# Kernel tuning notes

Hardware: AMD Instinct MI355X
Metric: run time of the kernel (lower is better)

## Reference

```python
import jax, jax.numpy as jnp
import numpy as np

N = 27          # num_classes (nodes)
C = 512         # in_channels
B = 64          # batch
L = 2           # layer_num
EPS = 1e-5


def setup_inputs() -> dict:
    key = jax.random.key(0)
    ks = jax.random.split(key, 7)
    scale = (2.0 / C) ** 0.5  # matches weight.data.normal_(0, sqrt(2/in_channels))
    mk = lambda k: jax.random.normal(k, (L, C, C), jnp.float32) * scale
    return {
        "x": jax.random.normal(ks[0], (B, N, C), jnp.float32),
        "edge": jax.random.normal(ks[1], (B, N * N, C), jnp.float32),
        "Wu": mk(ks[2]),
        "Wv": mk(ks[3]),
        "Wa": mk(ks[4]),
        "Wb": mk(ks[5]),
        "We": mk(ks[6]),
        "bnv_w": jnp.ones((L, N), jnp.float32),
        "bnv_b": jnp.zeros((L, N), jnp.float32),
        "bne_w": jnp.ones((L, N * N), jnp.float32),
        "bne_b": jnp.zeros((L, N * N), jnp.float32),
    }


def _bn(t, w, b):
    # BatchNorm1d in training mode over [B, channels, C]-style layout:
    # input is [B, ch, C]; normalize over (batch, last) dims, biased variance.
    mean = jnp.mean(t, axis=(0, 2), keepdims=True)
    var = jnp.mean((t - mean) ** 2, axis=(0, 2), keepdims=True)
    return (t - mean) * jax.lax.rsqrt(var + EPS) * w[None, :, None] + b[None, :, None]


def _layer(x, edge, Wu, Wv, Wa, Wb, We, bnv_w, bnv_b, bne_w, bne_b):
    b = x.shape[0]
    # einsum('ev,bvc->bec', end, A(x)) == repeat each node i over its n outgoing rows
    Ax = jnp.repeat(x @ Wa.T, N, axis=1)            # [b, n*n, c]
    # einsum('ev,bvc->bec', start, B(x)) == tile all nodes n times
    Bx = jnp.tile(x @ Wb.T, (1, N, 1))              # [b, n*n, c]
    m = Ax + Bx + edge @ We.T
    edge = edge + jax.nn.relu(_bn(m, bne_w, bne_b))
    e = jax.nn.sigmoid(edge)
    # softmax over dim 2 of the [b, n, n, c] view
    e = jax.nn.softmax(e.reshape(b, N, N, C), axis=2).reshape(b, N * N, C)
    Ujx = jnp.tile(x @ Wv.T, (1, N, 1))             # start-gather of V(x)
    # einsum('ve,bec->bvc', end.T, .) == segment-sum over consecutive groups of n edges
    agg = (e * Ujx).reshape(b, N, N, C).sum(axis=2)  # [b, n, c]
    x = x @ Wu.T + agg / N
    x = x + jax.nn.relu(_bn(x, bnv_w, bnv_b))
    return x, edge


def reference(x, edge, Wu, Wv, Wa, Wb, We, bnv_w, bnv_b, bne_w, bne_b):
    for l in range(L):
        x, edge = _layer(x, edge, Wu[l], Wv[l], Wa[l], Wb[l], We[l],
                         bnv_w[l], bnv_b[l], bne_w[l], bne_b[l])
    return (x, edge)
```

## Files before the change

kernel.cpp:

```cpp
#include <hip/hip_runtime.h>
#include <math.h>

#define NN 27
#define NE 729
#define CC 512
#define BB 64
#define EPSV 1e-5f

#define XROWS (BB*NN)
#define EROWS (BB*NE)

typedef short s16x8 __attribute__((ext_vector_type(8)));
typedef float f32x4 __attribute__((ext_vector_type(4)));
typedef unsigned short bfu_t;

typedef const __attribute__((address_space(1))) void gv_t;
typedef __attribute__((address_space(3))) void lv_t;

static __device__ __forceinline__ bfu_t f2bu(float f) {
    __bf16 h = (__bf16)f;
    return __builtin_bit_cast(unsigned short, h);
}

__global__ __launch_bounds__(256)
void f2b(const float* __restrict__ src, bfu_t* __restrict__ dst, int n)
{
    int i = (blockIdx.x * 256 + threadIdx.x) * 8;
    if (i >= n) return;
    float4 a = *(const float4*)(src + i);
    float4 b = *(const float4*)(src + i + 4);
    s16x8 v;
    v[0] = (short)f2bu(a.x); v[1] = (short)f2bu(a.y);
    v[2] = (short)f2bu(a.z); v[3] = (short)f2bu(a.w);
    v[4] = (short)f2bu(b.x); v[5] = (short)f2bu(b.y);
    v[6] = (short)f2bu(b.z); v[7] = (short)f2bu(b.w);
    *(s16x8*)(dst + i) = v;
}

__global__ __launch_bounds__(256)
void gemm_mfma(const bfu_t* __restrict__ A, const bfu_t* __restrict__ W,
               float* __restrict__ out, int M, int ldo,
               const float* __restrict__ xW, int mode)
{
    __shared__ bfu_t As[128 * 32];
    __shared__ bfu_t Bs[128 * 32];

    const int t    = threadIdx.x;
    const int lane = t & 63;
    const int w    = t >> 6;
    const int bm   = blockIdx.x * 128;
    const int bn   = blockIdx.y * 128;
    const int wr   = (w >> 1) * 64;
    const int wc   = (w & 1) * 64;

    f32x4 acc[4][4];
    #pragma unroll
    for (int i = 0; i < 4; ++i)
        #pragma unroll
        for (int j = 0; j < 4; ++j) acc[i][j] = (f32x4){0.f, 0.f, 0.f, 0.f};

    const int r0 = w * 32 + (lane >> 2);
    const int r1 = r0 + 16;
    const int kc = (lane & 3) * 8;
    int ga0 = bm + r0; if (ga0 > M - 1) ga0 = M - 1;
    int ga1 = bm + r1; if (ga1 > M - 1) ga1 = M - 1;
    const bfu_t* a0 = A + (size_t)ga0 * CC + kc;
    const bfu_t* a1 = A + (size_t)ga1 * CC + kc;
    const bfu_t* w0 = W + (size_t)(bn + r0) * CC + kc;
    const bfu_t* w1 = W + (size_t)(bn + r1) * CC + kc;
    bfu_t* lA0 = As + (w * 2 + 0) * 512;
    bfu_t* lA1 = As + (w * 2 + 1) * 512;
    bfu_t* lB0 = Bs + (w * 2 + 0) * 512;
    bfu_t* lB1 = Bs + (w * 2 + 1) * 512;

    const int fra = wr + (lane & 15);
    const int frb = wc + (lane & 15);
    const int fk  = (lane >> 4) * 8;

    for (int kt = 0; kt < CC; kt += 32) {
        if (kt) __syncthreads();
        __builtin_amdgcn_global_load_lds((gv_t*)(a0 + kt), (lv_t*)lA0, 16, 0, 0);
        __builtin_amdgcn_global_load_lds((gv_t*)(a1 + kt), (lv_t*)lA1, 16, 0, 0);
        __builtin_amdgcn_global_load_lds((gv_t*)(w0 + kt), (lv_t*)lB0, 16, 0, 0);
        __builtin_amdgcn_global_load_lds((gv_t*)(w1 + kt), (lv_t*)lB1, 16, 0, 0);
        __syncthreads();

        s16x8 af[4], bfg[4];
        #pragma unroll
        for (int i = 0; i < 4; ++i)
            af[i] = *(const s16x8*)&As[(fra + i * 16) * 32 + fk];
        #pragma unroll
        for (int i = 0; i < 4; ++i)
            bfg[i] = *(const s16x8*)&Bs[(frb + i * 16) * 32 + fk];
        #pragma unroll
        for (int i = 0; i < 4; ++i)
            #pragma unroll
            for (int j = 0; j < 4; ++j)
                acc[i][j] = __builtin_amdgcn_mfma_f32_16x16x32_bf16(af[i], bfg[j], acc[i][j], 0, 0, 0);
    }

    const int crb = wr + ((lane >> 4) << 2);
    const int ccb = wc + (lane & 15);
    if (mode == 0) {
        #pragma unroll
        for (int mi = 0; mi < 4; ++mi) {
            #pragma unroll
            for (int q = 0; q < 4; ++q) {
                int row = bm + crb + mi * 16 + q;
                if (row >= M) continue;
                float* o = out + (size_t)row * ldo + bn + ccb;
                #pragma unroll
                for (int ni = 0; ni < 4; ++ni) o[ni * 16] = acc[mi][ni][q];
            }
        }
    } else {
        #pragma unroll
        for (int mi = 0; mi < 4; ++mi) {
            #pragma unroll
            for (int q = 0; q < 4; ++q) {
                int row = bm + crb + mi * 16 + q;
                if (row >= M) continue;
                int b  = row / NE;
                int e  = row - b * NE;
                int i2 = e / NN;
                int j2 = e - i2 * NN;
                const float* axp = xW + (size_t)(b * NN + i2) * 2048 + bn + ccb;
                const float* bxp = xW + (size_t)(b * NN + j2) * 2048 + 512 + bn + ccb;
                float* o = out + (size_t)row * CC + bn + ccb;
                #pragma unroll
                for (int ni = 0; ni < 4; ++ni)
                    o[ni * 16] = acc[mi][ni][q] + axp[ni * 16] + bxp[ni * 16];
            }
        }
    }
}

__global__ __launch_bounds__(256)
void bn_stats(const float* __restrict__ src, int nch,
              const float* __restrict__ w, const float* __restrict__ bias,
              float* __restrict__ ka, float* __restrict__ kb)
{
    const int ch = blockIdx.x;
    const int t  = threadIdx.x;
    const int sub = t >> 7;
    const int cf  = (t & 127) * 4;

    float s = 0.f, sq = 0.f;
    for (int b = 0; b < BB; b += 2) {
        const float* p = src + ((size_t)(b + sub) * nch + ch) * CC + cf;
        float4 v = *(const float4*)p;
        s  += v.x + v.y + v.z + v.w;
        sq += v.x*v.x + v.y*v.y + v.z*v.z + v.w*v.w;
    }
    #pragma unroll
    for (int off = 32; off; off >>= 1) {
        s  += __shfl_down(s, off);
        sq += __shfl_down(sq, off);
    }
    __shared__ float red[2][4];
    const int wid = t >> 6, lane = t & 63;
    if (lane == 0) { red[0][wid] = s; red[1][wid] = sq; }
    __syncthreads();
    if (t == 0) {
        s  = red[0][0] + red[0][1] + red[0][2] + red[0][3];
        sq = red[1][0] + red[1][1] + red[1][2] + red[1][3];
        const float inv = 1.f / (float)(BB * CC);
        float mean = s * inv;
        float var  = sq * inv - mean * mean;
        float r    = rsqrtf(var + EPSV);
        float kaw  = r * w[ch];
        ka[ch] = kaw;
        kb[ch] = bias[ch] - mean * kaw;
    }
}

__global__ __launch_bounds__(256)
void edge_update(const float* __restrict__ m, const float* __restrict__ ein,
                 float* __restrict__ eout, bfu_t* __restrict__ ebf,
                 const float* __restrict__ ka, const float* __restrict__ kb)
{
    const size_t idx = (size_t)blockIdx.x * blockDim.x + threadIdx.x;
    const size_t total = (size_t)EROWS * CC / 4;
    if (idx >= total) return;
    const int e = (int)((idx >> 7) % NE);
    const float a = ka[e], b = kb[e];
    float4 mv = ((const float4*)m)[idx];
    float4 ev = ((const float4*)ein)[idx];
    float4 o;
    o.x = ev.x + fmaxf(fmaf(mv.x, a, b), 0.f);
    o.y = ev.y + fmaxf(fmaf(mv.y, a, b), 0.f);
    o.z = ev.z + fmaxf(fmaf(mv.z, a, b), 0.f);
    o.w = ev.w + fmaxf(fmaf(mv.w, a, b), 0.f);
    ((float4*)eout)[idx] = o;
    ushort4 h;
    h.x = f2bu(o.x); h.y = f2bu(o.y); h.z = f2bu(o.z); h.w = f2bu(o.w);
    ((ushort4*)ebf)[idx] = h;
}

__global__ __launch_bounds__(512)
void agg_kernel(const float* __restrict__ edge, const float* __restrict__ xW,
                float* __restrict__ xpre)
{
    const int bi = blockIdx.x;
    const int c  = threadIdx.x;
    const int b  = bi / NN;
    const int i  = bi - b * NN;

    const float* ebase = edge + ((size_t)b * NE + (size_t)i * NN) * CC + c;
    float ex[NN];
    float den = 0.f;
    #pragma unroll
    for (int j = 0; j < NN; ++j) {
        float sv  = ebase[(size_t)j * CC];
        float sig = 1.f / (1.f + __expf(-sv));
        float e   = __expf(sig);
        ex[j] = e;
        den  += e;
    }
    float accv = 0.f;
    const float* vbase = xW + (size_t)(b * NN) * 2048 + 1024 + c;
    #pragma unroll
    for (int j = 0; j < NN; ++j)
        accv = fmaf(ex[j], vbase[(size_t)j * 2048], accv);

    float u = xW[(size_t)bi * 2048 + 1536 + c];
    xpre[(size_t)bi * CC + c] = u + accv / (den * (float)NN);
}

__global__ __launch_bounds__(256)
void x_update(const float* __restrict__ xpre, float* __restrict__ xout,
              bfu_t* __restrict__ xbf,
              const float* __restrict__ ka, const float* __restrict__ kb)
{
    const int idx = blockIdx.x * blockDim.x + threadIdx.x;
    const int total = XROWS * CC / 4;
    if (idx >= total) return;
    const int i = (idx >> 7) % NN;
    const float a = ka[i], b = kb[i];
    float4 v = ((const float4*)xpre)[idx];
    float4 o;
    o.x = v.x + fmaxf(fmaf(v.x, a, b), 0.f);
    o.y = v.y + fmaxf(fmaf(v.y, a, b), 0.f);
    o.z = v.z + fmaxf(fmaf(v.z, a, b), 0.f);
    o.w = v.w + fmaxf(fmaf(v.w, a, b), 0.f);
    ((float4*)xout)[idx] = o;
    ushort4 h;
    h.x = f2bu(o.x); h.y = f2bu(o.y); h.z = f2bu(o.z); h.w = f2bu(o.w);
    ((ushort4*)xbf)[idx] = h;
}

extern "C" void kernel_launch(void* const* d_in, const int* in_sizes, int n_in,
                              void* d_out, int out_size, void* d_ws, size_t ws_size,
                              hipStream_t stream)
{
    const float* x0   = (const float*)d_in[0];
    const float* e0   = (const float*)d_in[1];
    const float* Wu   = (const float*)d_in[2];
    const float* Wv   = (const float*)d_in[3];
    const float* Wa   = (const float*)d_in[4];
    const float* Wb   = (const float*)d_in[5];
    const float* We   = (const float*)d_in[6];
    const float* bnvw = (const float*)d_in[7];
    const float* bnvb = (const float*)d_in[8];
    const float* bnew = (const float*)d_in[9];
    const float* bneb = (const float*)d_in[10];

    const size_t XSZ = (size_t)XROWS * CC;
    const size_t ESZ = (size_t)EROWS * CC;
    const int    WSZ = CC * CC;

    float* xout = (float*)d_out;
    float* eout = xout + XSZ;

    float* ws   = (float*)d_ws;
    float* xW   = ws;
    float* m    = xW + (size_t)XROWS * 2048;
    float* xpre = m + ESZ;
    float* ka_e = xpre + XSZ;
    float* kb_e = ka_e + NE;
    float* ka_v = kb_e + NE;
    float* kb_v = ka_v + NN;
    bfu_t* bws  = (bfu_t*)(ka_v + 2048);
    bfu_t* ebf  = bws;
    bfu_t* xbf  = ebf + ESZ;
    bfu_t* WnB  = xbf + XSZ;
    bfu_t* WeB  = WnB + (size_t)2 * 2048 * CC;

    const int wgrid = WSZ / 8 / 256;
    for (int l = 0; l < 2; ++l) {
        bfu_t* nb = WnB + (size_t)l * 2048 * CC;
        f2b<<<wgrid, 256, 0, stream>>>(Wa + (size_t)l * WSZ, nb,            WSZ);
        f2b<<<wgrid, 256, 0, stream>>>(Wb + (size_t)l * WSZ, nb + WSZ,      WSZ);
        f2b<<<wgrid, 256, 0, stream>>>(Wv + (size_t)l * WSZ, nb + 2 * WSZ,  WSZ);
        f2b<<<wgrid, 256, 0, stream>>>(Wu + (size_t)l * WSZ, nb + 3 * WSZ,  WSZ);
        f2b<<<wgrid, 256, 0, stream>>>(We + (size_t)l * WSZ, WeB + (size_t)l * WSZ, WSZ);
    }

    const dim3 gN(14, 16);
    const dim3 gE(365, 4);

    for (int l = 0; l < 2; ++l) {
        const float* ei = l ? (const float*)eout : e0;
        if (l == 0) {
            f2b<<<(int)(XSZ / 8 / 256), 256, 0, stream>>>(x0, xbf, (int)XSZ);
            f2b<<<(int)(ESZ / 8 / 256), 256, 0, stream>>>(e0, ebf, (int)ESZ);
        }

        gemm_mfma<<<gN, 256, 0, stream>>>(xbf, WnB + (size_t)l * 2048 * CC,
                                          xW, XROWS, 2048, nullptr, 0);
        gemm_mfma<<<gE, 256, 0, stream>>>(ebf, WeB + (size_t)l * WSZ,
                                          m, EROWS, CC, xW, 1);

        bn_stats<<<NE, 256, 0, stream>>>(m, NE, bnew + (size_t)l * NE,
                                         bneb + (size_t)l * NE, ka_e, kb_e);
        edge_update<<<(int)(ESZ / 4 / 256), 256, 0, stream>>>(m, ei, eout, ebf, ka_e, kb_e);

        agg_kernel<<<XROWS, 512, 0, stream>>>(eout, xW, xpre);

        bn_stats<<<NN, 256, 0, stream>>>(xpre, NN, bnvw + (size_t)l * NN,
                                         bnvb + (size_t)l * NN, ka_v, kb_v);
        x_update<<<(int)(XSZ / 4 / 256), 256, 0, stream>>>(xpre, xout, xbf, ka_v, kb_v);
    }
}
```

Baseline: 572.0 us.

## Fuse BN statistics into GEMM epilogue and merge edge update with aggregation

Edge BatchNorm sums and sums of squares are now accumulated with atomics inside the edge GEMM epilogue, which removes the separate bn_stats pass over the large m tensor. The edge update (BN, relu, residual, bf16 copy) is fused into the softmax-aggregation kernel, so the new edge is consumed straight from registers instead of being re-read. Node BN statistics are likewise accumulated with atomics in that kernel and turned into scale and shift inside x_update. All bf16 conversions are merged into one launch. The atomics add contention and make float summation order nondeterministic.

Result: slower. 642.7 us (+12.4%).

```diff
diff --git a/kernel.cpp b/kernel.cpp
--- a/kernel.cpp
+++ b/kernel.cpp
@@ -6,14 +6,13 @@
 #define CC 512
 #define BB 64
 #define EPSV 1e-5f
-
 #define XROWS (BB*NN)
 #define EROWS (BB*NE)
+#define WSZ   (CC*CC)
 
 typedef short s16x8 __attribute__((ext_vector_type(8)));
 typedef float f32x4 __attribute__((ext_vector_type(4)));
 typedef unsigned short bfu_t;
-
 typedef const __attribute__((address_space(1))) void gv_t;
 typedef __attribute__((address_space(3))) void lv_t;
 
@@ -23,24 +22,58 @@
 }
 
 __global__ __launch_bounds__(256)
-void f2b(const float* __restrict__ src, bfu_t* __restrict__ dst, int n)
-{
-    int i = (blockIdx.x * 256 + threadIdx.x) * 8;
-    if (i >= n) return;
-    float4 a = *(const float4*)(src + i);
-    float4 b = *(const float4*)(src + i + 4);
+void zero_stats(float* __restrict__ p)
+{
+    p[blockIdx.x * 256 + threadIdx.x] = 0.f;
+}
+
+__global__ __launch_bounds__(256)
+void convert_all(const float* __restrict__ Wa, const float* __restrict__ Wb,
+                 const float* __restrict__ Wv, const float* __restrict__ Wu,
+                 const float* __restrict__ We, const float* __restrict__ x0,
+                 const float* __restrict__ e0,
+                 bfu_t* __restrict__ WnB, bfu_t* __restrict__ WeB,
+                 bfu_t* __restrict__ xbf, bfu_t* __restrict__ ebf)
+{
+    const long i = (long)(blockIdx.x * 256 + threadIdx.x) * 8;
+    const long WTOT = 10L * WSZ;
+    const long XTOT = WTOT + (long)XROWS * CC;
+    const float* src;
+    bfu_t* dst;
+    if (i < WTOT) {
+        int  c   = (int)(i >> 18);
+        long off = i & (WSZ - 1);
+        if (c < 8) {
+            int l = c >> 2, t = c & 3;
+            const float* b = (t == 0) ? Wa : (t == 1) ? Wb : (t == 2) ? Wv : Wu;
+            src = b + (long)l * WSZ + off;
+            dst = WnB + (long)c * WSZ + off;
+        } else {
+            src = We + (long)(c - 8) * WSZ + off;
+            dst = WeB + (long)(c - 8) * WSZ + off;
+        }
+    } else if (i < XTOT) {
+        long off = i - WTOT;
+        src = x0 + off;  dst = xbf + off;
+    } else {
+        long off = i - XTOT;
+        src = e0 + off;  dst = ebf + off;
+    }
+    float4 a = *(const float4*)src;
+    float4 b = *(const float4*)(src + 4);
     s16x8 v;
     v[0] = (short)f2bu(a.x); v[1] = (short)f2bu(a.y);
     v[2] = (short)f2bu(a.z); v[3] = (short)f2bu(a.w);
     v[4] = (short)f2bu(b.x); v[5] = (short)f2bu(b.y);
     v[6] = (short)f2bu(b.z); v[7] = (short)f2bu(b.w);
-    *(s16x8*)(dst + i) = v;
+    *(s16x8*)dst = v;
 }
 
 __global__ __launch_bounds__(256)
 void gemm_mfma(const bfu_t* __restrict__ A, const bfu_t* __restrict__ W,
                float* __restrict__ out, int M, int ldo,
-               const float* __restrict__ xW, int mode)
+               const float* __restrict__ xW, int mode,
+               float* __restrict__ esum, float* __restrict__ esumsq)
 {
     __shared__ bfu_t As[128 * 32];
     __shared__ bfu_t Bs[128 * 32];
@@ -127,116 +160,120 @@
                 const float* axp = xW + (size_t)(b * NN + i2) * 2048 + bn + ccb;
                 const float* bxp = xW + (size_t)(b * NN + j2) * 2048 + 512 + bn + ccb;
                 float* o = out + (size_t)row * CC + bn + ccb;
+                float s = 0.f, sq = 0.f;
                 #pragma unroll
-                for (int ni = 0; ni < 4; ++ni)
-                    o[ni * 16] = acc[mi][ni][q] + axp[ni * 16] + bxp[ni * 16];
+                for (int ni = 0; ni < 4; ++ni) {
+                    float v = acc[mi][ni][q] + axp[ni * 16] + bxp[ni * 16];
+                    o[ni * 16] = v;
+                    s += v; sq += v * v;
+                }
+                #pragma unroll
+                for (int off = 1; off < 16; off <<= 1) {
+                    s  += __shfl_xor(s, off);
+                    sq += __shfl_xor(sq, off);
+                }
+                if ((lane & 15) == 0) {
+                    atomicAdd(&esum[e], s);
+                    atomicAdd(&esumsq[e], sq);
+                }
             }
         }
     }
 }
 
 __global__ __launch_bounds__(256)
-void bn_stats(const float* __restrict__ src, int nch,
-              const float* __restrict__ w, const float* __restrict__ bias,
-              float* __restrict__ ka, float* __restrict__ kb)
-{
-    const int ch = blockIdx.x;
-    const int t  = threadIdx.x;
-    const int sub = t >> 7;
-    const int cf  = (t & 127) * 4;
-
-    float s = 0.f, sq = 0.f;
-    for (int b = 0; b < BB; b += 2) {
-        const float* p = src + ((size_t)(b + sub) * nch + ch) * CC + cf;
-        float4 v = *(const float4*)p;
-        s  += v.x + v.y + v.z + v.w;
-        sq += v.x*v.x + v.y*v.y + v.z*v.z + v.w*v.w;
-    }
+void agg_edge(const float* __restrict__ m, const float* __restrict__ ein,
+              float* __restrict__ eout, bfu_t* __restrict__ ebf,
+              const float* __restrict__ xW, float* __restrict__ xpre,
+              const float* __restrict__ esum, const float* __restrict__ esumsq,
+              const float* __restrict__ bnew, const float* __restrict__ bneb,
+              float* __restrict__ vsum, float* __restrict__ vsumsq)
+{
+    const int bi = blockIdx.x;
+    const int b  = bi / NN;
+    const int i  = bi - b * NN;
+    const int c  = threadIdx.x * 2;
+
+    __shared__ float kae[NN], kbe[NN];
+    if (threadIdx.x < NN) {
+        int e = i * NN + threadIdx.x;
+        const float inv = 1.f / (float)(BB * CC);
+        float mean = esum[e] * inv;
+        float var  = esumsq[e] * inv - mean * mean;
+        float r    = rsqrtf(var + EPSV);
+        float a    = r * bnew[e];
+        kae[threadIdx.x] = a;
+        kbe[threadIdx.x] = bneb[e] - mean * a;
+    }
+    __syncthreads();
+
+    const size_t ebase = ((size_t)b * NE + (size_t)i * NN) * CC + c;
+    float2 ex[NN];
+    float2 den = {0.f, 0.f};
+    #pragma unroll
+    for (int j = 0; j < NN; ++j) {
+        size_t idx = ebase + (size_t)j * CC;
+        float2 mv = *(const float2*)(m + idx);
+        float2 ev = *(const float2*)(ein + idx);
+        float a = kae[j], bb = kbe[j];
+        float2 o;
+        o.x = ev.x + fmaxf(fmaf(mv.x, a, bb), 0.f);
+        o.y = ev.y + fmaxf(fmaf(mv.y, a, bb), 0.f);
+        *(float2*)(eout + idx) = o;
+        ushort2 h; h.x = f2bu(o.x); h.y = f2bu(o.y);
+        *(ushort2*)(ebf + idx) = h;
+        float sx = 1.f / (1.f + __expf(-o.x));
+        float sy = 1.f / (1.f + __expf(-o.y));
+        float gx = __expf(sx), gy = __expf(sy);
+        ex[j].x = gx; ex[j].y = gy;
+        den.x += gx; den.y += gy;
+    }
+
+    float2 accv = {0.f, 0.f};
+    const float* vb = xW + (size_t)(b * NN) * 2048 + 1024 + c;
+    #pragma unroll
+    for (int j = 0; j < NN; ++j) {
+        float2 v = *(const float2*)(vb + (size_t)j * 2048);
+        accv.x = fmaf(ex[j].x, v.x, accv.x);
+        accv.y = fmaf(ex[j].y, v.y, accv.y);
+    }
+    float2 u = *(const float2*)(xW + (size_t)bi * 2048 + 1536 + c);
+    float2 xp;
+    xp.x = u.x + accv.x / (den.x * (float)NN);
+    xp.y = u.y + accv.y / (den.y * (float)NN);
+    *(float2*)(xpre + (size_t)bi * CC + c) = xp;
+
+    float s  = xp.x + xp.y;
+    float sq = xp.x * xp.x + xp.y * xp.y;
     #pragma unroll
     for (int off = 32; off; off >>= 1) {
         s  += __shfl_down(s, off);
         sq += __shfl_down(sq, off);
     }
-    __shared__ float red[2][4];
-    const int wid = t >> 6, lane = t & 63;
-    if (lane == 0) { red[0][wid] = s; red[1][wid] = sq; }
+    __shared__ float rs[4], rq[4];
+    const int wid = threadIdx.x >> 6, lane = threadIdx.x & 63;
+    if (lane == 0) { rs[wid] = s; rq[wid] = sq; }
     __syncthreads();
-    if (t == 0) {
-        s  = red[0][0] + red[0][1] + red[0][2] + red[0][3];
-        sq = red[1][0] + red[1][1] + red[1][2] + red[1][3];
-        const float inv = 1.f / (float)(BB * CC);
-        float mean = s * inv;
-        float var  = sq * inv - mean * mean;
-        float r    = rsqrtf(var + EPSV);
-        float kaw  = r * w[ch];
-        ka[ch] = kaw;
-        kb[ch] = bias[ch] - mean * kaw;
-    }
-}
-
-__global__ __launch_bounds__(256)
-void edge_update(const float* __restrict__ m, const float* __restrict__ ein,
-                 float* __restrict__ eout, bfu_t* __restrict__ ebf,
-                 const float* __restrict__ ka, const float* __restrict__ kb)
-{
-    const size_t idx = (size_t)blockIdx.x * blockDim.x + threadIdx.x;
-    const size_t total = (size_t)EROWS * CC / 4;
-    if (idx >= total) return;
-    const int e = (int)((idx >> 7) % NE);
-    const float a = ka[e], b = kb[e];
-    float4 mv = ((const float4*)m)[idx];
-    float4 ev = ((const float4*)ein)[idx];
-    float4 o;
-    o.x = ev.x + fmaxf(fmaf(mv.x, a, b), 0.f);
-    o.y = ev.y + fmaxf(fmaf(mv.y, a, b), 0.f);
-    o.z = ev.z + fmaxf(fmaf(mv.z, a, b), 0.f);
-    o.w = ev.w + fmaxf(fmaf(mv.w, a, b), 0.f);
-    ((float4*)eout)[idx] = o;
-    ushort4 h;
-    h.x = f2bu(o.x); h.y = f2bu(o.y); h.z = f2bu(o.z); h.w = f2bu(o.w);
-    ((ushort4*)ebf)[idx] = h;
-}
-
-__global__ __launch_bounds__(512)
-void agg_kernel(const float* __restrict__ edge, const float* __restrict__ xW,
-                float* __restrict__ xpre)
-{
-    const int bi = blockIdx.x;
-    const int c  = threadIdx.x;
-    const int b  = bi / NN;
-    const int i  = bi - b * NN;
-
-    const float* ebase = edge + ((size_t)b * NE + (size_t)i * NN) * CC + c;
-    float ex[NN];
-    float den = 0.f;
-    #pragma unroll
-    for (int j = 0; j < NN; ++j) {
-        float sv  = ebase[(size_t)j * CC];
-        float sig = 1.f / (1.f + __expf(-sv));
-        float e   = __expf(sig);
-        ex[j] = e;
-        den  += e;
-    }
-    float accv = 0.f;
-    const float* vbase = xW + (size_t)(b * NN) * 2048 + 1024 + c;
-    #pragma unroll
-    for (int j = 0; j < NN; ++j)
-        accv = fmaf(ex[j], vbase[(size_t)j * 2048], accv);
-
-    float u = xW[(size_t)bi * 2048 + 1536 + c];
-    xpre[(size_t)bi * CC + c] = u + accv / (den * (float)NN);
+    if (threadIdx.x == 0) {
+        atomicAdd(&vsum[i],   rs[0] + rs[1] + rs[2] + rs[3]);
+        atomicAdd(&vsumsq[i], rq[0] + rq[1] + rq[2] + rq[3]);
+    }
 }
 
 __global__ __launch_bounds__(256)
 void x_update(const float* __restrict__ xpre, float* __restrict__ xout,
               bfu_t* __restrict__ xbf,
-              const float* __restrict__ ka, const float* __restrict__ kb)
-{
-    const int idx = blockIdx.x * blockDim.x + threadIdx.x;
-    const int total = XROWS * CC / 4;
-    if (idx >= total) return;
+              const float* __restrict__ vsum, const float* __restrict__ vsumsq,
+              const float* __restrict__ bnvw, const float* __restrict__ bnvb)
+{
+    const int idx = blockIdx.x * 256 + threadIdx.x;
     const int i = (idx >> 7) % NN;
-    const float a = ka[i], b = kb[i];
+    const float inv = 1.f / (float)(BB * CC);
+    float mean = vsum[i] * inv;
+    float var  = vsumsq[i] * inv - mean * mean;
+    float r    = rsqrtf(var + EPSV);
+    float a    = r * bnvw[i];
+    float b    = bnvb[i] - mean * a;
     float4 v = ((const float4*)xpre)[idx];
     float4 o;
     o.x = v.x + fmaxf(fmaf(v.x, a, b), 0.f);
@@ -267,58 +304,51 @@
 
     const size_t XSZ = (size_t)XROWS * CC;
     const size_t ESZ = (size_t)EROWS * CC;
-    const int    WSZ = CC * CC;
 
     float* xout = (float*)d_out;
     float* eout = xout + XSZ;
 
-    float* ws   = (float*)d_ws;
-    float* xW   = ws;
-    float* m    = xW + (size_t)XROWS * 2048;
-    float* xpre = m + ESZ;
-    float* ka_e = xpre + XSZ;
-    float* kb_e = ka_e + NE;
-    float* ka_v = kb_e + NE;
-    float* kb_v = ka_v + NN;
-    bfu_t* bws  = (bfu_t*)(ka_v + 2048);
-    bfu_t* ebf  = bws;
-    bfu_t* xbf  = ebf + ESZ;
-    bfu_t* WnB  = xbf + XSZ;
-    bfu_t* WeB  = WnB + (size_t)2 * 2048 * CC;
-
-    const int wgrid = WSZ / 8 / 256;
-    for (int l = 0; l < 2; ++l) {
-        bfu_t* nb = WnB + (size_t)l * 2048 * CC;
-        f2b<<<wgrid, 256, 0, stream>>>(Wa + (size_t)l * WSZ, nb,            WSZ);
-        f2b<<<wgrid, 256, 0, stream>>>(Wb + (size_t)l * WSZ, nb + WSZ,      WSZ);
-        f2b<<<wgrid, 256, 0, stream>>>(Wv + (size_t)l * WSZ, nb + 2 * WSZ,  WSZ);
-        f2b<<<wgrid, 256, 0, stream>>>(Wu + (size_t)l * WSZ, nb + 3 * WSZ,  WSZ);
-        f2b<<<wgrid, 256, 0, stream>>>(We + (size_t)l * WSZ, WeB + (size_t)l * WSZ, WSZ);
-    }
+    float* ws    = (float*)d_ws;
+    float* xW    = ws;
+    float* m     = xW + (size_t)XROWS * 2048;
+    float* xpre  = m + ESZ;
+    float* stats = xpre + XSZ;
+    float* esum  = stats;
+    float* esumsq = stats + NE;
+    float* vsum   = stats + 2 * NE;
+    float* vsumsq = stats + 2 * NE + NN;
+    bfu_t* bws = (bfu_t*)(stats + 1536);
+    bfu_t* ebf = bws;
+    bfu_t* xbf = ebf + ESZ;
+    bfu_t* WnB = xbf + XSZ;
+    bfu_t* WeB = WnB + (size_t)2 * 2048 * CC;
+
+    const long CTOT = 10L * WSZ + (long)XSZ + (long)ESZ;
+    convert_all<<<(int)(CTOT / 8 / 256), 256, 0, stream>>>(
+        Wa, Wb, Wv, Wu, We, x0, e0, WnB, WeB, xbf, ebf);
 
     const dim3 gN(14, 16);
     const dim3 gE(365, 4);
 
     for (int l = 0; l < 2; ++l) {
         const float* ei = l ? (const float*)eout : e0;
-        if (l == 0) {
-            f2b<<<(int)(XSZ / 8 / 256), 256, 0, stream>>>(x0, xbf, (int)XSZ);
-            f2b<<<(int)(ESZ / 8 / 256), 256, 0, stream>>>(e0, ebf, (int)ESZ);
-        }
-
-        gemm_mfma<<<gN, 256, 0, stream>>>(xbf, WnB + (size_t)l * 2048 * CC,
-                                          xW, XROWS, 2048, nullptr, 0);
+
+        zero_stats<<<6, 256, 0, stream>>>(stats);
+
+        gemm_mfma<<<gN, 256, 0, stream>>>(xbf, WnB + (size_t)l * 4 * WSZ,
+                                          xW, XROWS, 2048, nullptr, 0,
+                                          nullptr, nullptr);
         gemm_mfma<<<gE, 256, 0, stream>>>(ebf, WeB + (size_t)l * WSZ,
-                                          m, EROWS, CC, xW, 1);
-
-        bn_stats<<<NE, 256, 0, stream>>>(m, NE, bnew + (size_t)l * NE,
-                                         bneb + (size_t)l * NE, ka_e, kb_e);
-        edge_update<<<(int)(ESZ / 4 / 256), 256, 0, stream>>>(m, ei, eout, ebf, ka_e, kb_e);
-
-        agg_kernel<<<XROWS, 512, 0, stream>>>(eout, xW, xpre);
-
-        bn_stats<<<NN, 256, 0, stream>>>(xpre, NN, bnvw + (size_t)l * NN,
-                                         bnvb + (size_t)l * NN, ka_v, kb_v);
-        x_update<<<(int)(XSZ / 4 / 256), 256, 0, stream>>>(xpre, xout, xbf, ka_v, kb_v);
-    }
-}
+                                          m, EROWS, CC, xW, 1, esum, esumsq);
+
+        agg_edge<<<XROWS, 256, 0, stream>>>(m, ei, eout, ebf, xW, xpre,
+                                            esum, esumsq,
+                                            bnew + (size_t)l * NE,
+                                            bneb + (size_t)l * NE,
+                                            vsum, vsumsq);
+
+        x_update<<<(int)(XSZ / 4 / 256), 256, 0, stream>>>(
+            xpre, xout, xbf, vsum, vsumsq,
+            bnvw + (size_t)l * NN, bnvb + (size_t)l * NN);
+    }
+}
```
